# Optimization experiments

Measured on AMD Instinct MI355X. Metric: run time of the kernel, lower is better.

Reference implementation:

```python
import jax, jax.numpy as jnp
import numpy as np

N_FEATURES = 1024
N_OUTPUTS = 512
N = 32768
N_DECISIONS = 3  # root + 2 internal nodes (depth-2 tree)
N_LEAVES = 4


def setup_inputs() -> dict:
    key = jax.random.key(0)
    k_x, k_dw, k_db, k_lw, k_lb = jax.random.split(key, 5)
    xs = jax.random.normal(k_x, (N, N_FEATURES), dtype=jnp.float32)
    # decision hyperplanes for nodes [root, left-child, right-child]
    dec_w = jax.random.normal(k_dw, (N_DECISIONS, N_FEATURES), dtype=jnp.float32) / np.sqrt(N_FEATURES)
    dec_b = jax.random.normal(k_db, (N_DECISIONS,), dtype=jnp.float32) * 0.01
    # linear leaves, ordered [LL, LR, RL, RR]
    leaf_w = jax.random.normal(k_lw, (N_LEAVES, N_FEATURES, N_OUTPUTS), dtype=jnp.float32) / np.sqrt(N_FEATURES)
    leaf_b = jax.random.normal(k_lb, (N_LEAVES, N_OUTPUTS), dtype=jnp.float32) * 0.01
    return {"xs": xs, "dec_w": dec_w, "dec_b": dec_b, "leaf_w": leaf_w, "leaf_b": leaf_b}


def reference(xs, dec_w, dec_b, leaf_w, leaf_b):
    # decisions at all 3 branch nodes: [N, 3] boolean (True -> go right)
    d = (xs @ dec_w.T + dec_b) > 0
    d0, d1, d2 = d[:, 0], d[:, 1], d[:, 2]
    # leaf index per sample: root False -> left subtree (node 1), True -> right subtree (node 2)
    leaf_idx = jnp.where(
        d0,
        jnp.where(d2, 3, 2),
        jnp.where(d1, 1, 0),
    )  # [N]
    # compute all leaf outputs densely (equivalent math to masked dispatch), then select
    outs = jnp.einsum("nf,kfd->nkd", xs, leaf_w) + leaf_b  # [N, 4, D]
    out = jnp.take_along_axis(outs, leaf_idx[:, None, None], axis=1)[:, 0]  # [N, D]
    return out
```

## Files before the change

### kernel.cpp

```cpp
#include <hip/hip_runtime.h>
#include <hip/hip_bf16.h>
#include <stdint.h>

#define NROWS 32768
#define NFEAT 1024
#define NOUT  512

typedef __attribute__((ext_vector_type(8))) short bf16x8;
typedef __attribute__((ext_vector_type(4))) float f32x4;

#define WS_CNT  0
#define WS_LIST 256
#define WS_BT   524544
#define WS_XB   (WS_BT + (size_t)4 * NOUT * NFEAT * 2)
#define WS_NEEDED (WS_XB + (size_t)NROWS * NFEAT * 2)

#define NDEC_BLOCKS 1024
#define NTR_BLOCKS  512

__global__ __launch_bounds__(64) void zero_cnt_kernel(int* __restrict__ cnt) {
  if (threadIdx.x < 4) cnt[threadIdx.x] = 0;
}

__global__ __launch_bounds__(256) void decide_tr_kernel(
    const float* __restrict__ xs, const float* __restrict__ dw,
    const float* __restrict__ db, const float* __restrict__ lw,
    __hip_bfloat16* __restrict__ bt, int* __restrict__ cnt,
    int* __restrict__ list, __hip_bfloat16* __restrict__ xsb ) {
  __shared__ float smem[32 * 33];
  const int tid = threadIdx.x;
  int b = blockIdx.x;

  if (b >= NDEC_BLOCKS) {
    int tb = b - NDEC_BLOCKS;
    int l = tb >> 7;
    int t = tb & 127;
    int d0 = (t >> 3) * 32;
    int k00 = (t & 7) * 128;
    int x = tid & 31, y = tid >> 5;
    const float* src = lw + (size_t)l * NFEAT * NOUT;
    __hip_bfloat16* dst = bt + (size_t)l * NOUT * NFEAT;
    float (*tile)[33] = (float(*)[33])smem;
    for (int kk = 0; kk < 4; ++kk) {
      int k0 = k00 + kk * 32;
#pragma unroll
      for (int i = 0; i < 4; ++i)
        tile[y * 4 + i][x] = src[(size_t)(k0 + y * 4 + i) * NOUT + d0 + x];
      __syncthreads();
#pragma unroll
      for (int i = 0; i < 4; ++i)
        dst[(size_t)(d0 + y * 4 + i) * NFEAT + k0 + x] =
            __float2bfloat16(tile[x][y * 4 + i]);
      __syncthreads();
    }
    return;
  }

  int* leaf_of = (int*)smem;
  const int lane = tid & 63;
  const int wv = tid >> 6;

  f32x4 w0[4], w1[4], w2[4];
#pragma unroll
  for (int c = 0; c < 2; ++c)
#pragma unroll
    for (int h = 0; h < 2; ++h) {
      int idx = c * 512 + lane * 8 + h * 4;
      w0[c * 2 + h] = *(const f32x4*)(dw + idx);
      w1[c * 2 + h] = *(const f32x4*)(dw + NFEAT + idx);
      w2[c * 2 + h] = *(const f32x4*)(dw + 2 * NFEAT + idx);
    }
  float b0 = db[0], b1 = db[1], b2 = db[2];

  int rowbase = b * 32 + wv * 8;
  for (int r = 0; r < 8; ++r) {
    int row = rowbase + r;
    const float* xr = xs + (size_t)row * NFEAT;
    float s0 = 0.f, s1 = 0.f, s2 = 0.f;
#pragma unroll
    for (int c = 0; c < 2; ++c) {
      int idx = c * 512 + lane * 8;
      f32x4 xv0 = *(const f32x4*)(xr + idx);
      f32x4 xv1 = *(const f32x4*)(xr + idx + 4);
#pragma unroll
      for (int j = 0; j < 4; ++j) {
        s0 += xv0[j] * w0[c * 2][j] + xv1[j] * w0[c * 2 + 1][j];
        s1 += xv0[j] * w1[c * 2][j] + xv1[j] * w1[c * 2 + 1][j];
        s2 += xv0[j] * w2[c * 2][j] + xv1[j] * w2[c * 2 + 1][j];
      }
      if (xsb) {
        union { bf16x8 v; __hip_bfloat16 h[8]; } pk;
#pragma unroll
        for (int j = 0; j < 4; ++j) {
          pk.h[j] = __float2bfloat16(xv0[j]);
          pk.h[j + 4] = __float2bfloat16(xv1[j]);
        }
        *(bf16x8*)(xsb + (size_t)row * NFEAT + idx) = pk.v;
      }
    }
#pragma unroll
    for (int off = 32; off > 0; off >>= 1) {
      s0 += __shfl_xor(s0, off);
      s1 += __shfl_xor(s1, off);
      s2 += __shfl_xor(s2, off);
    }
    if (lane == 0) {
      int lf = (s0 + b0 > 0.f) ? ((s2 + b2 > 0.f) ? 3 : 2)
                               : ((s1 + b1 > 0.f) ? 1 : 0);
      leaf_of[wv * 8 + r] = lf;
    }
  }
  __syncthreads();

  if (tid < 64) {
    int i = tid;
    int myleaf = (i < 32) ? leaf_of[i] : -1;
    int myrow = b * 32 + i;
    unsigned long long m0 = __ballot(myleaf == 0);
    unsigned long long m1 = __ballot(myleaf == 1);
    unsigned long long m2 = __ballot(myleaf == 2);
    unsigned long long m3 = __ballot(myleaf == 3);
    unsigned long long mym = (myleaf == 0) ? m0 : (myleaf == 1) ? m1
                           : (myleaf == 2) ? m2 : (myleaf == 3) ? m3 : 0ull;
    unsigned long long below = (1ull << i) - 1ull;
    int rank = __popcll(mym & below);
    int base = 0;
    if (i < 4) {
      unsigned long long mi = (i == 0) ? m0 : (i == 1) ? m1 : (i == 2) ? m2 : m3;
      base = atomicAdd(&cnt[i], __popcll(mi));
    }
    int mybase = __shfl(base, (myleaf < 0) ? 0 : myleaf);
    if (i < 32) list[myleaf * NROWS + mybase + rank] = myrow;
  }
}

#define BM 128
#define BN 128
#define BK 64
#define KSTEPS (NFEAT / BK)

__device__ __forceinline__ bool decode_tile(const int* cnt, int& leaf, int& mloc,
                                            int& ntile, int& cc) {
  int bid = blockIdx.x;
  int cpx = (int)(gridDim.x >> 3);
  int swz = (bid & 7) * cpx + (bid >> 3);
  int mtile = swz >> 2;
  ntile = swz & 3;
  int c0 = cnt[0], c1 = cnt[1], c2 = cnt[2], c3 = cnt[3];
  int t0 = (c0 + BM - 1) / BM, t1 = (c1 + BM - 1) / BM;
  int t2 = (c2 + BM - 1) / BM, t3 = (c3 + BM - 1) / BM;
  if (mtile < t0)                     { leaf = 0; mloc = mtile;                cc = c0; }
  else if (mtile < t0 + t1)           { leaf = 1; mloc = mtile - t0;           cc = c1; }
  else if (mtile < t0 + t1 + t2)      { leaf = 2; mloc = mtile - t0 - t1;      cc = c2; }
  else if (mtile < t0 + t1 + t2 + t3) { leaf = 3; mloc = mtile - t0 - t1 - t2; cc = c3; }
  else return false;
  return true;
}

__global__ __launch_bounds__(256, 2) void gemm_db_kernel(
    const __hip_bfloat16* __restrict__ xsb, const __hip_bfloat16* __restrict__ bt,
    const float* __restrict__ lb, const int* __restrict__ cnt,
    const int* __restrict__ list, float* __restrict__ out) {
  __shared__ __hip_bfloat16 Al[2][BM * BK];
  __shared__ __hip_bfloat16 Bl[2][BN * BK];
  __shared__ int rows_s[BM];

  int leaf, mloc, ntile, cc;
  if (!decode_tile(cnt, leaf, mloc, ntile, cc)) return;

  const int tid = threadIdx.x;
  if (tid < BM) {
    int i = mloc * BM + tid;
    rows_s[tid] = (i < cc) ? list[leaf * NROWS + i] : -1;
  }
  __syncthreads();

  const int lane = tid & 63;
  const int wv = tid >> 6;
  const int g8 = (((lane & 7) ^ (lane >> 3)) << 3);
  const __hip_bfloat16* asrc[4];
  const __hip_bfloat16* bsrc[4];
#pragma unroll
  for (int j = 0; j < 4; ++j) {
    int tr = wv * 32 + j * 8 + (lane >> 3);
    int grow = rows_s[tr];
    if (grow < 0) grow = 0;
    asrc[j] = xsb + (size_t)grow * NFEAT + g8;
    bsrc[j] = bt + ((size_t)leaf * NOUT + ntile * BN + tr) * NFEAT + g8;
  }

#define STAGE(BUF, KS)                                                       \
  {                                                                          \
    _Pragma("unroll") for (int j = 0; j < 4; ++j) {                          \
      __builtin_amdgcn_global_load_lds(                                      \
          (const __attribute__((address_space(1))) void*)(asrc[j] + (KS) * BK), \
          (__attribute__((address_space(3))) void*)(&Al[BUF][(wv * 4 + j) * 512]), \
          16, 0, 0);                                                         \
      __builtin_amdgcn_global_load_lds(                                      \
          (const __attribute__((address_space(1))) void*)(bsrc[j] + (KS) * BK), \
          (__attribute__((address_space(3))) void*)(&Bl[BUF][(wv * 4 + j) * 512]), \
          16, 0, 0);                                                         \
    }                                                                        \
  }

  const int wr = (wv >> 1) * 64;
  const int wc = (wv & 1) * 64;
  f32x4 acc[4][4];
#pragma unroll
  for (int m = 0; m < 4; ++m)
#pragma unroll
    for (int n = 0; n < 4; ++n) acc[m][n] = (f32x4){0.f, 0.f, 0.f, 0.f};

  STAGE(0, 0);
  __syncthreads();

  int cur = 0;
  for (int ks = 0; ks < KSTEPS; ++ks) {
    if (ks + 1 < KSTEPS) {
      if (cur == 0) STAGE(1, ks + 1) else STAGE(0, ks + 1);
    }

    const __hip_bfloat16* Ac = Al[cur];
    const __hip_bfloat16* Bc = Bl[cur];
#pragma unroll
    for (int kk = 0; kk < 2; ++kk) {
      bf16x8 af[4], bfr[4];
      int gk = kk * 4 + (lane >> 4);
#pragma unroll
      for (int m = 0; m < 4; ++m) {
        int r = wr + m * 16 + (lane & 15);
        af[m] = *(const bf16x8*)(&Ac[r * BK + ((gk ^ (r & 7)) << 3)]);
      }
#pragma unroll
      for (int n = 0; n < 4; ++n) {
        int r = wc + n * 16 + (lane & 15);
        bfr[n] = *(const bf16x8*)(&Bc[r * BK + ((gk ^ (r & 7)) << 3)]);
      }
#pragma unroll
      for (int m = 0; m < 4; ++m)
#pragma unroll
        for (int n = 0; n < 4; ++n)
          acc[m][n] = __builtin_amdgcn_mfma_f32_16x16x32_bf16(
              af[m], bfr[n], acc[m][n], 0, 0, 0);
    }
    __syncthreads();
    cur ^= 1;
  }

  int colb = ntile * BN + wc;
#pragma unroll
  for (int n = 0; n < 4; ++n) {
    int col = colb + n * 16 + (lane & 15);
    float bias = lb[leaf * NOUT + col];
#pragma unroll
    for (int m = 0; m < 4; ++m) {
#pragma unroll
      for (int r = 0; r < 4; ++r) {
        int lrow = wr + m * 16 + (lane >> 4) * 4 + r;
        int grow = rows_s[lrow];
        if (grow >= 0) out[(size_t)grow * NOUT + col] = acc[m][n][r] + bias;
      }
    }
  }
}

__global__ __launch_bounds__(256) void gemm_fallback_kernel(
    const float* __restrict__ xs, const __hip_bfloat16* __restrict__ bt,
    const float* __restrict__ lb, const int* __restrict__ cnt,
    const int* __restrict__ list, float* __restrict__ out) {
  __shared__ __hip_bfloat16 Afl[BM * BK];
  __shared__ __hip_bfloat16 Bfl[BN * BK];
  __shared__ int rows_s[BM];

  int leaf, mloc, ntile, cc;
  if (!decode_tile(cnt, leaf, mloc, ntile, cc)) return;

  const int tid = threadIdx.x;
  if (tid < BM) {
    int i = mloc * BM + tid;
    rows_s[tid] = (i < cc) ? list[leaf * NROWS + i] : -1;
  }
  __syncthreads();

  const int srow = tid >> 1;
  const int shalf = tid & 1;
  int a_grow = rows_s[srow];
  int a_clamp = (a_grow < 0) ? 0 : a_grow;
  const float* aptr = xs + (size_t)a_clamp * NFEAT + shalf * 32;
  const __hip_bfloat16* bptr =
      bt + ((size_t)leaf * NOUT + ntile * BN + srow) * NFEAT + shalf * 32;

  const int lane = tid & 63;
  const int wv = tid >> 6;
  const int wr = (wv >> 1) * 64;
  const int wc = (wv & 1) * 64;

  f32x4 acc[4][4];
#pragma unroll
  for (int m = 0; m < 4; ++m)
#pragma unroll
    for (int n = 0; n < 4; ++n) acc[m][n] = (f32x4){0.f, 0.f, 0.f, 0.f};

  f32x4 av[8];
  bf16x8 bv[4];
#define LOAD_TILE(K0)                                                        \
  {                                                                          \
    _Pragma("unroll") for (int j = 0; j < 8; ++j)                            \
        av[j] = *(const f32x4*)(aptr + (K0) + j * 4);                        \
    _Pragma("unroll") for (int j = 0; j < 4; ++j)                            \
        bv[j] = *(const bf16x8*)(bptr + (K0) + j * 8);                       \
  }

  LOAD_TILE(0);

  for (int ks = 0; ks < KSTEPS; ++ks) {
#pragma unroll
    for (int j = 0; j < 4; ++j) {
      union { bf16x8 v; __hip_bfloat16 h[8]; } pk;
#pragma unroll
      for (int e = 0; e < 8; ++e)
        pk.h[e] = __float2bfloat16(av[j * 2 + (e >> 2)][e & 3]);
      int g = shalf * 4 + j;
      *(bf16x8*)(&Afl[srow * BK + ((g ^ (srow & 7)) << 3)]) = pk.v;
    }
#pragma unroll
    for (int j = 0; j < 4; ++j) {
      int g = shalf * 4 + j;
      *(bf16x8*)(&Bfl[srow * BK + ((g ^ (srow & 7)) << 3)]) = bv[j];
    }
    __syncthreads();

    if (ks + 1 < KSTEPS) LOAD_TILE((ks + 1) * BK);

#pragma unroll
    for (int kk = 0; kk < 2; ++kk) {
      bf16x8 af[4], bfr[4];
      int gk = kk * 4 + (lane >> 4);
#pragma unroll
      for (int m = 0; m < 4; ++m) {
        int r = wr + m * 16 + (lane & 15);
        af[m] = *(const bf16x8*)(&Afl[r * BK + ((gk ^ (r & 7)) << 3)]);
      }
#pragma unroll
      for (int n = 0; n < 4; ++n) {
        int r = wc + n * 16 + (lane & 15);
        bfr[n] = *(const bf16x8*)(&Bfl[r * BK + ((gk ^ (r & 7)) << 3)]);
      }
#pragma unroll
      for (int m = 0; m < 4; ++m)
#pragma unroll
        for (int n = 0; n < 4; ++n)
          acc[m][n] = __builtin_amdgcn_mfma_f32_16x16x32_bf16(
              af[m], bfr[n], acc[m][n], 0, 0, 0);
    }
    __syncthreads();
  }

  int colb = ntile * BN + wc;
#pragma unroll
  for (int n = 0; n < 4; ++n) {
    int col = colb + n * 16 + (lane & 15);
    float bias = lb[leaf * NOUT + col];
#pragma unroll
    for (int m = 0; m < 4; ++m) {
#pragma unroll
      for (int r = 0; r < 4; ++r) {
        int lrow = wr + m * 16 + (lane >> 4) * 4 + r;
        int grow = rows_s[lrow];
        if (grow >= 0) out[(size_t)grow * NOUT + col] = acc[m][n][r] + bias;
      }
    }
  }
}

extern "C" void kernel_launch(void* const* d_in, const int* in_sizes, int n_in,
                              void* d_out, int out_size, void* d_ws, size_t ws_size,
                              hipStream_t stream) {
  const float* xs = (const float*)d_in[0];
  const float* dw = (const float*)d_in[1];
  const float* db = (const float*)d_in[2];
  const float* lw = (const float*)d_in[3];
  const float* lb = (const float*)d_in[4];
  float* out = (float*)d_out;
  char* ws = (char*)d_ws;
  int* cnt = (int*)(ws + WS_CNT);
  int* list = (int*)(ws + WS_LIST);
  __hip_bfloat16* bt = (__hip_bfloat16*)(ws + WS_BT);
  bool big = ws_size >= WS_NEEDED;
  __hip_bfloat16* xsb = big ? (__hip_bfloat16*)(ws + WS_XB) : nullptr;

  zero_cnt_kernel<<<1, 64, 0, stream>>>(cnt);
  decide_tr_kernel<<<NDEC_BLOCKS + NTR_BLOCKS, 256, 0, stream>>>(
      xs, dw, db, lw, bt, cnt, list, xsb);
  if (big)
    gemm_db_kernel<<<1040, 256, 0, stream>>>(xsb, bt, lb, cnt, list, out);
  else
    gemm_fallback_kernel<<<1040, 256, 0, stream>>>(xs, bt, lb, cnt, list, out);
}
```

Before: 114.8 us.

## Restructure GEMM double-buffer pipeline with explicit vmcnt waits and MFMA priority

Replaces the syncthreads-based double buffer in the leaf GEMM with an explicit pipeline. Two stages are prefetched up front, and each step waits with s_waitcnt vmcnt(8) so the next stage's global-to-LDS loads stay in flight. The buffer just consumed is refilled two steps ahead, after a barrier. It also raises wave priority around the MFMA block and adds sched_barriers to pin the instruction order. The aim is to hide global load latency behind compute. The cost is relying on hand-counted vmcnt values and ordering that the compiler can no longer adjust.

```diff
diff --git a/kernel.cpp b/kernel.cpp
--- a/kernel.cpp
+++ b/kernel.cpp
@@ -157,7 +157,7 @@
   return true;
 }
 
-__global__ __launch_bounds__(256, 2) void gemm_db_kernel(
+__global__ __launch_bounds__(256, 2) void gemm_cnt_kernel(
     const __hip_bfloat16* __restrict__ xsb, const __hip_bfloat16* __restrict__ bt,
     const float* __restrict__ lb, const int* __restrict__ cnt,
     const int* __restrict__ list, float* __restrict__ out) {
@@ -211,17 +211,24 @@
 #pragma unroll
     for (int n = 0; n < 4; ++n) acc[m][n] = (f32x4){0.f, 0.f, 0.f, 0.f};
 
+  asm volatile("s_waitcnt vmcnt(0)" ::: "memory");
+  __builtin_amdgcn_sched_barrier(0);
   STAGE(0, 0);
-  __syncthreads();
+  STAGE(1, 1);
 
   int cur = 0;
   for (int ks = 0; ks < KSTEPS; ++ks) {
-    if (ks + 1 < KSTEPS) {
-      if (cur == 0) STAGE(1, ks + 1) else STAGE(0, ks + 1);
-    }
-
-    const __hip_bfloat16* Ac = Al[cur];
-    const __hip_bfloat16* Bc = Bl[cur];
+    if (ks < KSTEPS - 1) {
+      asm volatile("s_waitcnt vmcnt(8)" ::: "memory");
+    } else {
+      asm volatile("s_waitcnt vmcnt(0)" ::: "memory");
+    }
+    __builtin_amdgcn_sched_barrier(0);
+    __builtin_amdgcn_s_barrier();
+    __builtin_amdgcn_sched_barrier(0);
+
+    const __hip_bfloat16* Ac = &Al[cur][0];
+    const __hip_bfloat16* Bc = &Bl[cur][0];
 #pragma unroll
     for (int kk = 0; kk < 2; ++kk) {
       bf16x8 af[4], bfr[4];
@@ -236,14 +243,22 @@
         int r = wc + n * 16 + (lane & 15);
         bfr[n] = *(const bf16x8*)(&Bc[r * BK + ((gk ^ (r & 7)) << 3)]);
       }
+      asm volatile("s_waitcnt lgkmcnt(0)" ::: "memory");
+      __builtin_amdgcn_sched_barrier(0);
+      __builtin_amdgcn_s_setprio(1);
 #pragma unroll
       for (int m = 0; m < 4; ++m)
 #pragma unroll
         for (int n = 0; n < 4; ++n)
           acc[m][n] = __builtin_amdgcn_mfma_f32_16x16x32_bf16(
               af[m], bfr[n], acc[m][n], 0, 0, 0);
-    }
-    __syncthreads();
+      __builtin_amdgcn_s_setprio(0);
+      __builtin_amdgcn_sched_barrier(0);
+    }
+
+    __builtin_amdgcn_s_barrier();
+    __builtin_amdgcn_sched_barrier(0);
+    if (ks + 2 < KSTEPS) STAGE(cur, ks + 2);
     cur ^= 1;
   }
 
@@ -393,7 +408,7 @@
   decide_tr_kernel<<<NDEC_BLOCKS + NTR_BLOCKS, 256, 0, stream>>>(
       xs, dw, db, lw, bt, cnt, list, xsb);
   if (big)
-    gemm_db_kernel<<<1040, 256, 0, stream>>>(xsb, bt, lb, cnt, list, out);
+    gemm_cnt_kernel<<<1040, 256, 0, stream>>>(xsb, bt, lb, cnt, list, out);
   else
     gemm_fallback_kernel<<<1040, 256, 0, stream>>>(xs, bt, lb, cnt, list, out);
 }
```

After: 124.8 us. +8.7%, slower.

## Replace LDS-staged leaf GEMM with register-direct MFMA fragment loads

Applied to the files above, without the earlier changes.

The gathered leaf GEMM used to stage 128x128 tiles through double-buffered LDS with a barrier after every k-step. It now uses 256x64 tiles, and each wave loads its MFMA A and B fragments straight from global memory into registers with a two-phase prefetch. This removes LDS traffic and barriers. In exchange there is no cross-wave reuse, since each wave rereads the same B fragments and A rows from global memory or L2, so the kernel depends more on cache bandwidth.

```diff
diff --git a/kernel.cpp b/kernel.cpp
--- a/kernel.cpp
+++ b/kernel.cpp
@@ -134,10 +134,114 @@
   }
 }
 
+#define BK 64
+#define KSTEPS (NFEAT / BK)
+
+#define BMR 256
+
+__global__ __launch_bounds__(256, 2) void gemm_reg_kernel(
+    const __hip_bfloat16* __restrict__ xsb, const __hip_bfloat16* __restrict__ bt,
+    const float* __restrict__ lb, const int* __restrict__ cnt,
+    const int* __restrict__ list, float* __restrict__ out) {
+  __shared__ int rows_s[BMR];
+
+  int bid = blockIdx.x;
+  int cpx = (int)(gridDim.x >> 3);
+  int swz = (bid & 7) * cpx + (bid >> 3);
+  int mtile = swz >> 3;
+  int nslice = swz & 7;
+  int c0 = cnt[0], c1 = cnt[1], c2 = cnt[2], c3 = cnt[3];
+  int t0 = (c0 + BMR - 1) / BMR, t1 = (c1 + BMR - 1) / BMR;
+  int t2 = (c2 + BMR - 1) / BMR, t3 = (c3 + BMR - 1) / BMR;
+  int leaf, mloc, cc;
+  if (mtile < t0)                     { leaf = 0; mloc = mtile;                cc = c0; }
+  else if (mtile < t0 + t1)           { leaf = 1; mloc = mtile - t0;           cc = c1; }
+  else if (mtile < t0 + t1 + t2)      { leaf = 2; mloc = mtile - t0 - t1;      cc = c2; }
+  else if (mtile < t0 + t1 + t2 + t3) { leaf = 3; mloc = mtile - t0 - t1 - t2; cc = c3; }
+  else return;
+
+  const int tid = threadIdx.x;
+  {
+    int i = mloc * BMR + tid;
+    rows_s[tid] = (i < cc) ? list[leaf * NROWS + i] : -1;
+  }
+  __syncthreads();
+
+  const int lane = tid & 63;
+  const int wv = tid >> 6;
+  const int hi = lane >> 4;
+  const int lo = lane & 15;
+
+  const __hip_bfloat16* abase[4];
+#pragma unroll
+  for (int m = 0; m < 4; ++m) {
+    int grow = rows_s[wv * 64 + m * 16 + lo];
+    if (grow < 0) grow = 0;
+    abase[m] = xsb + (size_t)grow * NFEAT + hi * 8;
+  }
+  const __hip_bfloat16* bbase[4];
+#pragma unroll
+  for (int n = 0; n < 4; ++n) {
+    int bcol = nslice * 64 + n * 16 + lo;
+    bbase[n] = bt + ((size_t)leaf * NOUT + bcol) * NFEAT + hi * 8;
+  }
+
+  f32x4 acc[4][4];
+#pragma unroll
+  for (int m = 0; m < 4; ++m)
+#pragma unroll
+    for (int n = 0; n < 4; ++n) acc[m][n] = (f32x4){0.f, 0.f, 0.f, 0.f};
+
+  bf16x8 afr[2][4], bfr[2][4];
+
+#pragma unroll
+  for (int m = 0; m < 4; ++m) afr[0][m] = *(const bf16x8*)(abase[m]);
+#pragma unroll
+  for (int n = 0; n < 4; ++n) bfr[0][n] = *(const bf16x8*)(bbase[n]);
+
+#pragma unroll
+  for (int ks = 0; ks < KSTEPS; ++ks) {
+#pragma unroll
+    for (int kk = 0; kk < 2; ++kk) {
+      const int ph = (ks * 2 + kk) & 1;
+      const int np = ph ^ 1;
+      const int nxt_off = ks * 64 + kk * 32 + 32;
+      if (ks * 2 + kk + 1 < KSTEPS * 2) {
+#pragma unroll
+        for (int m = 0; m < 4; ++m)
+          afr[np][m] = *(const bf16x8*)(abase[m] + nxt_off);
+#pragma unroll
+        for (int n = 0; n < 4; ++n)
+          bfr[np][n] = *(const bf16x8*)(bbase[n] + nxt_off);
+      }
+#pragma unroll
+      for (int m = 0; m < 4; ++m)
+#pragma unroll
+        for (int n = 0; n < 4; ++n)
+          acc[m][n] = __builtin_amdgcn_mfma_f32_16x16x32_bf16(
+              afr[ph][m], bfr[ph][n], acc[m][n], 0, 0, 0);
+    }
+  }
+
+  int colb = nslice * 64;
+#pragma unroll
+  for (int n = 0; n < 4; ++n) {
+    int col = colb + n * 16 + lo;
+    float bias = lb[leaf * NOUT + col];
+#pragma unroll
+    for (int m = 0; m < 4; ++m) {
+#pragma unroll
+      for (int r = 0; r < 4; ++r) {
+        int lrow = wv * 64 + m * 16 + hi * 4 + r;
+        int grow = rows_s[lrow];
+        if (grow >= 0) out[(size_t)grow * NOUT + col] = acc[m][n][r] + bias;
+      }
+    }
+  }
+}
+
 #define BM 128
 #define BN 128
-#define BK 64
-#define KSTEPS (NFEAT / BK)
 
 __device__ __forceinline__ bool decode_tile(const int* cnt, int& leaf, int& mloc,
                                             int& ntile, int& cc) {
@@ -157,113 +261,6 @@
   return true;
 }
 
-__global__ __launch_bounds__(256, 2) void gemm_db_kernel(
-    const __hip_bfloat16* __restrict__ xsb, const __hip_bfloat16* __restrict__ bt,
-    const float* __restrict__ lb, const int* __restrict__ cnt,
-    const int* __restrict__ list, float* __restrict__ out) {
-  __shared__ __hip_bfloat16 Al[2][BM * BK];
-  __shared__ __hip_bfloat16 Bl[2][BN * BK];
-  __shared__ int rows_s[BM];
-
-  int leaf, mloc, ntile, cc;
-  if (!decode_tile(cnt, leaf, mloc, ntile, cc)) return;
-
-  const int tid = threadIdx.x;
-  if (tid < BM) {
-    int i = mloc * BM + tid;
-    rows_s[tid] = (i < cc) ? list[leaf * NROWS + i] : -1;
-  }
-  __syncthreads();
-
-  const int lane = tid & 63;
-  const int wv = tid >> 6;
-  const int g8 = (((lane & 7) ^ (lane >> 3)) << 3);
-  const __hip_bfloat16* asrc[4];
-  const __hip_bfloat16* bsrc[4];
-#pragma unroll
-  for (int j = 0; j < 4; ++j) {
-    int tr = wv * 32 + j * 8 + (lane >> 3);
-    int grow = rows_s[tr];
-    if (grow < 0) grow = 0;
-    asrc[j] = xsb + (size_t)grow * NFEAT + g8;
-    bsrc[j] = bt + ((size_t)leaf * NOUT + ntile * BN + tr) * NFEAT + g8;
-  }
-
-#define STAGE(BUF, KS)                                                       \
-  {                                                                          \
-    _Pragma("unroll") for (int j = 0; j < 4; ++j) {                          \
-      __builtin_amdgcn_global_load_lds(                                      \
-          (const __attribute__((address_space(1))) void*)(asrc[j] + (KS) * BK), \
-          (__attribute__((address_space(3))) void*)(&Al[BUF][(wv * 4 + j) * 512]), \
-          16, 0, 0);                                                         \
-      __builtin_amdgcn_global_load_lds(                                      \
-          (const __attribute__((address_space(1))) void*)(bsrc[j] + (KS) * BK), \
-          (__attribute__((address_space(3))) void*)(&Bl[BUF][(wv * 4 + j) * 512]), \
-          16, 0, 0);                                                         \
-    }                                                                        \
-  }
-
-  const int wr = (wv >> 1) * 64;
-  const int wc = (wv & 1) * 64;
-  f32x4 acc[4][4];
-#pragma unroll
-  for (int m = 0; m < 4; ++m)
-#pragma unroll
-    for (int n = 0; n < 4; ++n) acc[m][n] = (f32x4){0.f, 0.f, 0.f, 0.f};
-
-  STAGE(0, 0);
-  __syncthreads();
-
-  int cur = 0;
-  for (int ks = 0; ks < KSTEPS; ++ks) {
-    if (ks + 1 < KSTEPS) {
-      if (cur == 0) STAGE(1, ks + 1) else STAGE(0, ks + 1);
-    }
-
-    const __hip_bfloat16* Ac = Al[cur];
-    const __hip_bfloat16* Bc = Bl[cur];
-#pragma unroll
-    for (int kk = 0; kk < 2; ++kk) {
-      bf16x8 af[4], bfr[4];
-      int gk = kk * 4 + (lane >> 4);
-#pragma unroll
-      for (int m = 0; m < 4; ++m) {
-        int r = wr + m * 16 + (lane & 15);
-        af[m] = *(const bf16x8*)(&Ac[r * BK + ((gk ^ (r & 7)) << 3)]);
-      }
-#pragma unroll
-      for (int n = 0; n < 4; ++n) {
-        int r = wc + n * 16 + (lane & 15);
-        bfr[n] = *(const bf16x8*)(&Bc[r * BK + ((gk ^ (r & 7)) << 3)]);
-      }
-#pragma unroll
-      for (int m = 0; m < 4; ++m)
-#pragma unroll
-        for (int n = 0; n < 4; ++n)
-          acc[m][n] = __builtin_amdgcn_mfma_f32_16x16x32_bf16(
-              af[m], bfr[n], acc[m][n], 0, 0, 0);
-    }
-    __syncthreads();
-    cur ^= 1;
-  }
-
-  int colb = ntile * BN + wc;
-#pragma unroll
-  for (int n = 0; n < 4; ++n) {
-    int col = colb + n * 16 + (lane & 15);
-    float bias = lb[leaf * NOUT + col];
-#pragma unroll
-    for (int m = 0; m < 4; ++m) {
-#pragma unroll
-      for (int r = 0; r < 4; ++r) {
-        int lrow = wr + m * 16 + (lane >> 4) * 4 + r;
-        int grow = rows_s[lrow];
-        if (grow >= 0) out[(size_t)grow * NOUT + col] = acc[m][n][r] + bias;
-      }
-    }
-  }
-}
-
 __global__ __launch_bounds__(256) void gemm_fallback_kernel(
     const float* __restrict__ xs, const __hip_bfloat16* __restrict__ bt,
     const float* __restrict__ lb, const int* __restrict__ cnt,
@@ -392,8 +389,9 @@
   zero_cnt_kernel<<<1, 64, 0, stream>>>(cnt);
   decide_tr_kernel<<<NDEC_BLOCKS + NTR_BLOCKS, 256, 0, stream>>>(
       xs, dw, db, lw, bt, cnt, list, xsb);
-  if (big)
-    gemm_db_kernel<<<1040, 256, 0, stream>>>(xsb, bt, lb, cnt, list, out);
-  else
+  if (big) {
+    gemm_reg_kernel<<<1056, 256, 0, stream>>>(xsb, bt, lb, cnt, list, out);
+  } else {
     gemm_fallback_kernel<<<1040, 256, 0, stream>>>(xs, bt, lb, cnt, list, out);
-}
+  }
+}
```

Measured after the change: 228.9 us. 99.3% more time.
